# Kernel tuning notes

Hardware: AMD Instinct MI355X
Metric: run time of the kernel (lower is better)

## Reference

```python
import jax, jax.numpy as jnp
import numpy as np

B, IMG, P, C_IN, D, NH, DEPTH, E, TOPK, NCLS = 8, 224, 16, 3, 768, 12, 12, 8, 2, 1000
DH = 4 * D
HD = D // NH
GRID = IMG // P
NPAT = GRID * GRID
MOE_POS = (1, 3, 5, 7, 9, 11)
N_DENSE = DEPTH - len(MOE_POS)
N_MOE = len(MOE_POS)


def setup_inputs() -> dict:
    key = jax.random.key(0)
    ks = iter(jax.random.split(key, 32))
    n = lambda shape: jax.random.normal(next(ks), shape, jnp.float32) * 0.02
    return dict(
        x=jax.random.normal(next(ks), (B, C_IN, IMG, IMG), jnp.float32),
        patch_w=n((D, C_IN * P * P)), patch_b=jnp.zeros((D,), jnp.float32),
        cls_token=n((1, 1, D)), pos_embed=n((1, NPAT + 1, D)),
        ln1_w=jnp.ones((DEPTH, D), jnp.float32), ln1_b=jnp.zeros((DEPTH, D), jnp.float32),
        qkv_w=n((DEPTH, 3 * D, D)), qkv_b=jnp.zeros((DEPTH, 3 * D), jnp.float32),
        proj_w=n((DEPTH, D, D)), proj_b=jnp.zeros((DEPTH, D), jnp.float32),
        ln2_w=jnp.ones((DEPTH, D), jnp.float32), ln2_b=jnp.zeros((DEPTH, D), jnp.float32),
        fc1_w=n((N_DENSE, DH, D)), fc1_b=jnp.zeros((N_DENSE, DH), jnp.float32),
        fc2_w=n((N_DENSE, D, DH)), fc2_b=jnp.zeros((N_DENSE, D), jnp.float32),
        gate_w=n((N_MOE, E, D)), gate_b=jnp.zeros((N_MOE, E), jnp.float32),
        exp_w1=n((N_MOE, E, DH, D)), exp_b1=jnp.zeros((N_MOE, E, DH), jnp.float32),
        exp_w2=n((N_MOE, E, D, DH)), exp_b2=jnp.zeros((N_MOE, E, D), jnp.float32),
        norm_w=jnp.ones((D,), jnp.float32), norm_b=jnp.zeros((D,), jnp.float32),
        head_w=n((NCLS, D)), head_b=jnp.zeros((NCLS,), jnp.float32),
    )


def _ln(x, w, b):
    m = x.mean(-1, keepdims=True)
    v = ((x - m) ** 2).mean(-1, keepdims=True)
    return (x - m) / jnp.sqrt(v + 1e-5) * w + b


def _attn(x, qw, qb, pw, pb):
    Bn, N, _ = x.shape
    qkv = (x @ qw.T + qb).reshape(Bn, N, 3, NH, HD).transpose(2, 0, 3, 1, 4)
    q, k, v = qkv[0], qkv[1], qkv[2]  # [B, NH, N, HD]
    a = jax.nn.softmax(jnp.einsum('bhnd,bhmd->bhnm', q, k) * HD ** -0.5, -1)
    o = jnp.einsum('bhnm,bhmd->bhnd', a, v).transpose(0, 2, 1, 3).reshape(Bn, N, D)
    return o @ pw.T + pb


def _moe(x, gw, gb, w1, b1, w2, b2):
    # FMoETransformerMLP with NaiveGate: top-2 routing, softmax over top-k logits.
    shp = x.shape
    xf = x.reshape(-1, D)  # [T, D]
    logits = xf @ gw.T + gb  # [T, E]
    vals, idx = jax.lax.top_k(logits, TOPK)
    sc = jax.nn.softmax(vals, -1)  # [T, TOPK]
    comb = (jax.nn.one_hot(idx, E, dtype=xf.dtype) * sc[..., None]).sum(1)  # [T, E]
    h = jax.nn.gelu(jnp.einsum('td,ehd->teh', xf, w1) + b1, approximate=False)
    y = jnp.einsum('teh,edh->ted', h, w2) + b2
    return (y * comb[..., None]).sum(1).reshape(shp)


def reference(x, patch_w, patch_b, cls_token, pos_embed, ln1_w, ln1_b, qkv_w, qkv_b, proj_w, proj_b, ln2_w, ln2_b, fc1_w, fc1_b, fc2_w, fc2_b, gate_w, gate_b, exp_w1, exp_b1, exp_w2, exp_b2, norm_w, norm_b, head_w, head_b):
    patches = x.reshape(B, C_IN, GRID, P, GRID, P).transpose(0, 2, 4, 1, 3, 5).reshape(B, NPAT, C_IN * P * P)
    z = jnp.concatenate([jnp.broadcast_to(cls_token, (B, 1, D)), patches @ patch_w.T + patch_b], 1) + pos_embed
    di = mi = 0
    for i in range(DEPTH):
        z = z + _attn(_ln(z, ln1_w[i], ln1_b[i]), qkv_w[i], qkv_b[i], proj_w[i], proj_b[i])
        h2 = _ln(z, ln2_w[i], ln2_b[i])
        if i in MOE_POS:
            z = z + _moe(h2, gate_w[mi], gate_b[mi], exp_w1[mi], exp_b1[mi], exp_w2[mi], exp_b2[mi])
            mi += 1
        else:
            z = z + (jax.nn.gelu(h2 @ fc1_w[di].T + fc1_b[di], approximate=False) @ fc2_w[di].T + fc2_b[di])
            di += 1
    z = _ln(z, norm_w, norm_b)
    return z[:, 0] @ head_w.T + head_b
```

## Files before the change

### kernel.cpp

```cpp
#include <hip/hip_runtime.h>
#include <hip/hip_bf16.h>
#include <math.h>

#define B_     8
#define IMG_   224
#define PATCH_ 16
#define CIN_   3
#define D_     768
#define NH_    12
#define DEPTH_ 12
#define NE_    8
#define NCLS_  1000
#define DH_    3072
#define HD_    64
#define GRD_   14
#define NPAT_  196
#define NTOK_  197
#define T_     (B_*NTOK_)
#define TP_    (B_*NPAT_)
#define NSLOT_ (T_*2)

typedef __bf16 bf16_t;
typedef __bf16 bf16x8 __attribute__((ext_vector_type(8)));
typedef __bf16 bf16x4 __attribute__((ext_vector_type(4)));
typedef float  f32x4  __attribute__((ext_vector_type(4)));

static __device__ __forceinline__ float gelu_f(float x){
    return 0.5f * x * (1.0f + erff(x * 0.70710678118654752440f));
}

__global__ __launch_bounds__(256) void k_cvt(const float* __restrict__ in,
                                             bf16_t* __restrict__ out, int n){
    int i = (blockIdx.x*256 + threadIdx.x)*8;
    if (i >= n) return;
    float4 a = *reinterpret_cast<const float4*>(in + i);
    float4 b = *reinterpret_cast<const float4*>(in + i + 4);
    bf16x8 h;
    h[0]=(bf16_t)a.x; h[1]=(bf16_t)a.y; h[2]=(bf16_t)a.z; h[3]=(bf16_t)a.w;
    h[4]=(bf16_t)b.x; h[5]=(bf16_t)b.y; h[6]=(bf16_t)b.z; h[7]=(bf16_t)b.w;
    *reinterpret_cast<bf16x8*>(out + i) = h;
}

__global__ void k_patch_gather(const float* __restrict__ x, bf16_t* __restrict__ pbuf){
    int idx = blockIdx.x*256 + threadIdx.x;
    if (idx >= TP_*D_) return;
    int k  = idx % D_;
    int tp = idx / D_;
    int p  = tp % NPAT_, b = tp / NPAT_;
    int c  = k >> 8;
    int ij = k & 255;
    int i  = ij >> 4, j = ij & 15;
    int gi = p / GRD_, gj = p % GRD_;
    pbuf[idx] = (bf16_t)x[(((size_t)b*CIN_ + c)*IMG_ + gi*PATCH_ + i)*IMG_ + gj*PATCH_ + j];
}

template<int ACT, int RES, int GATHER, int MOE, int OUTBF>
__global__ __launch_bounds__(256) void k_mgemm(
    const bf16_t* __restrict__ A, const int* __restrict__ gidx,
    const bf16_t* __restrict__ W, const float* __restrict__ bias,
    const float* __restrict__ res, void* __restrict__ Cout,
    int M, int N, int K,
    const int* __restrict__ moff, const int* __restrict__ mcnt)
{
    __shared__ __align__(16) bf16_t As[2][64*64];
    __shared__ __align__(16) bf16_t Bs[2][128*64];
    const int tid = threadIdx.x, lane = tid & 63, w = tid >> 6;
    int row_begin, Mhi;
    if (MOE) {
        const int e = blockIdx.z;
        const int o = moff[e], c = mcnt[e];
        row_begin = o + blockIdx.y*64;
        Mhi = o + c;
        if (row_begin >= Mhi) return;
        W    += (size_t)e*N*K;
        bias += (size_t)e*N;
    } else {
        row_begin = blockIdx.y*64;
        Mhi = M;
    }
    const int bn = blockIdx.x*128;

    const bf16_t* aG[2];
    const bf16_t* wG[4];
    int aOff[2], wOff[4];
    #pragma unroll
    for (int i = 0; i < 2; ++i) {
        const int s = w*2 + i;
        const int row_l = s*8 + (lane >> 3);
        const int cc = (lane & 7) ^ (row_l & 7);
        const int gg = min(row_begin + row_l, Mhi - 1);
        const int tok = GATHER ? (gidx[gg] >> 1) : gg;
        aG[i] = A + (size_t)tok*K + cc*8;
        aOff[i] = s*512;
    }
    #pragma unroll
    for (int j = 0; j < 4; ++j) {
        const int s = w*4 + j;
        const int row_l = s*8 + (lane >> 3);
        const int cc = (lane & 7) ^ (row_l & 7);
        wG[j] = W + (size_t)(bn + row_l)*K + cc*8;
        wOff[j] = s*512;
    }
    const int wm = (w >> 1)*32, wn = (w & 1)*64;
    const int fr = lane & 15, kg = lane >> 4;
    int offA[2][2], offB[2][4];
    #pragma unroll
    for (int ks = 0; ks < 2; ++ks) {
        #pragma unroll
        for (int t = 0; t < 2; ++t) {
            const int ra = wm + t*16 + fr;
            offA[ks][t] = ra*128 + (((ks*4 + kg) ^ (ra & 7)) << 4);
        }
        #pragma unroll
        for (int t = 0; t < 4; ++t) {
            const int rb = wn + t*16 + fr;
            offB[ks][t] = rb*128 + (((ks*4 + kg) ^ (rb & 7)) << 4);
        }
    }

    f32x4 acc[2][4] = {};
    const int nt = K >> 6;
    int cur = 0;
    #pragma unroll
    for (int i = 0; i < 2; ++i) {
        __builtin_amdgcn_global_load_lds(
            (const __attribute__((address_space(1))) void*)(aG[i]),
            (__attribute__((address_space(3))) void*)(&As[0][aOff[i]]), 16, 0, 0);
        aG[i] += 64;
    }
    #pragma unroll
    for (int j = 0; j < 4; ++j) {
        __builtin_amdgcn_global_load_lds(
            (const __attribute__((address_space(1))) void*)(wG[j]),
            (__attribute__((address_space(3))) void*)(&Bs[0][wOff[j]]), 16, 0, 0);
        wG[j] += 64;
    }
    __syncthreads();
    for (int t = 0; t < nt; ++t) {
        if (t + 1 < nt) {
            const int nb = cur ^ 1;
            #pragma unroll
            for (int i = 0; i < 2; ++i) {
                __builtin_amdgcn_global_load_lds(
                    (const __attribute__((address_space(1))) void*)(aG[i]),
                    (__attribute__((address_space(3))) void*)(&As[nb][aOff[i]]), 16, 0, 0);
                aG[i] += 64;
            }
            #pragma unroll
            for (int j = 0; j < 4; ++j) {
                __builtin_amdgcn_global_load_lds(
                    (const __attribute__((address_space(1))) void*)(wG[j]),
                    (__attribute__((address_space(3))) void*)(&Bs[nb][wOff[j]]), 16, 0, 0);
                wG[j] += 64;
            }
        }
        const char* baseA = (const char*)&As[cur][0];
        const char* baseB = (const char*)&Bs[cur][0];
        #pragma unroll
        for (int ks = 0; ks < 2; ++ks) {
            bf16x8 af[2], bf[4];
            #pragma unroll
            for (int t2 = 0; t2 < 2; ++t2)
                af[t2] = *reinterpret_cast<const bf16x8*>(baseA + offA[ks][t2]);
            #pragma unroll
            for (int t2 = 0; t2 < 4; ++t2)
                bf[t2] = *reinterpret_cast<const bf16x8*>(baseB + offB[ks][t2]);
            #pragma unroll
            for (int mt = 0; mt < 2; ++mt)
                #pragma unroll
                for (int nt2 = 0; nt2 < 4; ++nt2)
                    acc[mt][nt2] = __builtin_amdgcn_mfma_f32_16x16x32_bf16(
                        af[mt], bf[nt2], acc[mt][nt2], 0, 0, 0);
        }
        __syncthreads();
        cur ^= 1;
    }
    float*  Cf = (float*)Cout;
    bf16_t* Cb = (bf16_t*)Cout;
    const int cr = (lane >> 4)*4;
    #pragma unroll
    for (int nt2 = 0; nt2 < 4; ++nt2) {
        const int n = bn + wn + nt2*16 + fr;
        const float bv = bias[n];
        #pragma unroll
        for (int mt = 0; mt < 2; ++mt) {
            #pragma unroll
            for (int r2 = 0; r2 < 4; ++r2) {
                const int m = row_begin + wm + mt*16 + cr + r2;
                if (m < Mhi) {
                    float v = acc[mt][nt2][r2] + bv;
                    if (ACT) v = gelu_f(v);
                    if (RES) v += res[(size_t)m*N + n];
                    if (OUTBF) Cb[(size_t)m*N + n] = (bf16_t)v;
                    else       Cf[(size_t)m*N + n] = v;
                }
            }
        }
    }
}

struct LNOut { float y0, y1, y2; };
static __device__ __forceinline__ LNOut ln_block(float v0, float v1, float v2,
        const float* __restrict__ w, const float* __restrict__ b,
        float* red, int tid)
{
    const int wid = tid >> 6, lane = tid & 63;
    float s = v0 + v1 + v2;
    for (int m=32;m>0;m>>=1) s += __shfl_xor(s, m);
    if (lane == 0) red[wid] = s;
    __syncthreads();
    if (tid == 0) red[4] = (red[0]+red[1]+red[2]+red[3]) * (1.0f/768.0f);
    __syncthreads();
    const float mean = red[4];
    float d0 = v0-mean, d1 = v1-mean, d2 = v2-mean;
    float q = d0*d0 + d1*d1 + d2*d2;
    for (int m=32;m>0;m>>=1) q += __shfl_xor(q, m);
    if (lane == 0) red[wid] = q;
    __syncthreads();
    if (tid == 0) {
        float var = (red[0]+red[1]+red[2]+red[3]) * (1.0f/768.0f);
        red[5] = 1.0f / sqrtf(var + 1e-5f);
    }
    __syncthreads();
    const float rstd = red[5];
    LNOut o;
    o.y0 = d0*rstd*w[tid    ] + b[tid    ];
    o.y1 = d1*rstd*w[tid+256] + b[tid+256];
    o.y2 = d2*rstd*w[tid+512] + b[tid+512];
    return o;
}

template<typename TOUT>
__global__ __launch_bounds__(256) void k_ln(const float* __restrict__ X,
        const float* __restrict__ w, const float* __restrict__ b,
        TOUT* __restrict__ Y, int in_mul)
{
    __shared__ float red[8];
    const int r = blockIdx.x, tid = threadIdx.x;
    const float* xr = X + (size_t)r*in_mul*D_;
    LNOut o = ln_block(xr[tid], xr[tid+256], xr[tid+512], w, b, red, tid);
    TOUT* yr = Y + (size_t)r*D_;
    yr[tid] = (TOUT)o.y0; yr[tid+256] = (TOUT)o.y1; yr[tid+512] = (TOUT)o.y2;
}

__global__ __launch_bounds__(256) void k_asmln(const float* __restrict__ pe,
        const float* __restrict__ cls, const float* __restrict__ pos,
        float* __restrict__ z, const float* __restrict__ w,
        const float* __restrict__ b, bf16_t* __restrict__ Y)
{
    __shared__ float red[8];
    const int t = blockIdx.x, tid = threadIdx.x;
    const int bb = t / NTOK_, r = t % NTOK_;
    float v[3];
    #pragma unroll
    for (int j = 0; j < 3; ++j) {
        const int n = tid + j*256;
        if (r == 0) v[j] = cls[n] + pos[n];
        else        v[j] = pe[((size_t)bb*NPAT_ + (r-1))*D_ + n] + pos[(size_t)r*D_ + n];
        z[(size_t)t*D_ + n] = v[j];
    }
    LNOut o = ln_block(v[0], v[1], v[2], w, b, red, tid);
    bf16_t* yr = Y + (size_t)t*D_;
    yr[tid] = (bf16_t)o.y0; yr[tid+256] = (bf16_t)o.y1; yr[tid+512] = (bf16_t)o.y2;
}

__global__ __launch_bounds__(256) void k_lngate(const float* __restrict__ X,
        const float* __restrict__ w, const float* __restrict__ b,
        const float* __restrict__ gw, const float* __restrict__ gb,
        bf16_t* __restrict__ Y, int* __restrict__ t_e, float* __restrict__ t_sc)
{
    __shared__ float red[8];
    __shared__ float red2[4][8];
    const int t = blockIdx.x, tid = threadIdx.x;
    const int wid = tid >> 6, lane = tid & 63;
    const float* xr = X + (size_t)t*D_;
    LNOut o = ln_block(xr[tid], xr[tid+256], xr[tid+512], w, b, red, tid);
    bf16_t* yr = Y + (size_t)t*D_;
    yr[tid] = (bf16_t)o.y0; yr[tid+256] = (bf16_t)o.y1; yr[tid+512] = (bf16_t)o.y2;
    float p[NE_];
    #pragma unroll
    for (int e = 0; e < NE_; ++e)
        p[e] = o.y0*gw[e*D_+tid] + o.y1*gw[e*D_+tid+256] + o.y2*gw[e*D_+tid+512];
    #pragma unroll
    for (int e = 0; e < NE_; ++e)
        for (int m=32;m>0;m>>=1) p[e] += __shfl_xor(p[e], m);
    if (lane == 0)
        #pragma unroll
        for (int e = 0; e < NE_; ++e) red2[wid][e] = p[e];
    __syncthreads();
    if (tid == 0) {
        float l[NE_];
        #pragma unroll
        for (int e = 0; e < NE_; ++e)
            l[e] = red2[0][e]+red2[1][e]+red2[2][e]+red2[3][e] + gb[e];
        int i0 = 0;
        for (int e = 1; e < NE_; ++e) if (l[e] > l[i0]) i0 = e;
        int i1 = -1;
        for (int e = 0; e < NE_; ++e) if (e != i0 && (i1 < 0 || l[e] > l[i1])) i1 = e;
        float e1 = __expf(l[i1] - l[i0]);
        float s = 1.0f + e1;
        t_e[t*2]   = i0;   t_e[t*2+1]  = i1;
        t_sc[t*2]  = 1.0f/s; t_sc[t*2+1] = e1/s;
    }
}

__global__ __launch_bounds__(256) void k_scansc(const int* __restrict__ t_e,
        int* __restrict__ gidx, int* __restrict__ rg,
        int* __restrict__ offs, int* __restrict__ counts)
{
    __shared__ int h[NE_], o[NE_], c2[NE_];
    const int tid = threadIdx.x;
    if (tid < NE_) h[tid] = 0;
    __syncthreads();
    for (int id = tid; id < NSLOT_; id += 256) atomicAdd(&h[t_e[id]], 1);
    __syncthreads();
    if (tid == 0) {
        int s = 0;
        for (int e = 0; e < NE_; ++e) { o[e] = s; s += h[e]; c2[e] = 0; }
    }
    __syncthreads();
    if (tid < NE_) { offs[tid] = o[tid]; counts[tid] = h[tid]; }
    for (int id = tid; id < NSLOT_; id += 256) {
        int e = t_e[id];
        int pos = atomicAdd(&c2[e], 1);
        int g = o[e] + pos;
        gidx[g] = id;
        rg[id] = g;
    }
}

__global__ __launch_bounds__(256) void k_combln(const float* __restrict__ yb,
        const int* __restrict__ rg, const float* __restrict__ t_sc,
        float* __restrict__ z, const float* __restrict__ w,
        const float* __restrict__ b, bf16_t* __restrict__ Y)
{
    __shared__ float red[8];
    const int t = blockIdx.x, tid = threadIdx.x;
    const int g0 = rg[t*2], g1 = rg[t*2+1];
    const float s0 = t_sc[t*2], s1 = t_sc[t*2+1];
    float v[3];
    #pragma unroll
    for (int j = 0; j < 3; ++j) {
        const int n = tid + j*256;
        float nv = z[(size_t)t*D_+n] + s0*yb[(size_t)g0*D_+n] + s1*yb[(size_t)g1*D_+n];
        z[(size_t)t*D_+n] = nv;
        v[j] = nv;
    }
    LNOut o = ln_block(v[0], v[1], v[2], w, b, red, tid);
    bf16_t* yr = Y + (size_t)t*D_;
    yr[tid] = (bf16_t)o.y0; yr[tid+256] = (bf16_t)o.y1; yr[tid+512] = (bf16_t)o.y2;
}

__global__ void k_combine(const float* __restrict__ yb, const int* __restrict__ rg,
                          const float* __restrict__ t_sc, float* __restrict__ z){
    int idx = blockIdx.x*256 + threadIdx.x;
    if (idx >= T_*D_) return;
    int t = idx / D_, n = idx % D_;
    int g0 = rg[t*2], g1 = rg[t*2+1];
    z[idx] += t_sc[t*2]*yb[(size_t)g0*D_+n] + t_sc[t*2+1]*yb[(size_t)g1*D_+n];
}

__global__ __launch_bounds__(256) void k_attn(const bf16_t* __restrict__ qkv,
                                              bf16_t* __restrict__ out)
{
    __shared__ bf16_t Kl[NTOK_*68];
    __shared__ float  qs[8][64];
    __shared__ bf16_t ps[8][200];
    const int qb = blockIdx.x*8;
    const int h = blockIdx.y, b = blockIdx.z;
    const int tid = threadIdx.x, lane = tid & 63, wid = tid >> 6;
    for (int id = tid; id < NTOK_*8; id += 256) {
        const int m = id >> 3, c = id & 7;
        bf16x8 v = *reinterpret_cast<const bf16x8*>(
            qkv + (size_t)(b*NTOK_+m)*2304 + 768 + h*HD_ + c*8);
        bf16x4 lo = {v[0],v[1],v[2],v[3]}, hi = {v[4],v[5],v[6],v[7]};
        *reinterpret_cast<bf16x4*>(&Kl[m*68 + c*8    ]) = lo;
        *reinterpret_cast<bf16x4*>(&Kl[m*68 + c*8 + 4]) = hi;
    }
    for (int id = tid; id < 512; id += 256) {
        const int qq = id >> 6, d = id & 63;
        const int n = qb + qq;
        qs[qq][d] = (n < NTOK_) ? (float)qkv[(size_t)(b*NTOK_+n)*2304 + h*HD_ + d] : 0.0f;
    }
    __syncthreads();
    const int na = qb + wid, nb = qb + wid + 4;
    const bool va = na < NTOK_, vb = nb < NTOK_;
    if (!va) return;
    float sa[4] = {0,0,0,0}, sb[4] = {0,0,0,0};
    for (int d = 0; d < HD_; d += 4) {
        const f32x4 qa = *reinterpret_cast<const f32x4*>(&qs[wid][d]);
        const f32x4 qv = *reinterpret_cast<const f32x4*>(&qs[wid+4][d]);
        #pragma unroll
        for (int j = 0; j < 4; ++j) {
            const int m = lane + 64*j;
            const int mc = m < NTOK_ ? m : NTOK_-1;
            bf16x4 kv = *reinterpret_cast<const bf16x4*>(&Kl[mc*68 + d]);
            float k0=(float)kv[0], k1=(float)kv[1], k2=(float)kv[2], k3=(float)kv[3];
            sa[j] += qa[0]*k0 + qa[1]*k1 + qa[2]*k2 + qa[3]*k3;
            sb[j] += qv[0]*k0 + qv[1]*k1 + qv[2]*k2 + qv[3]*k3;
        }
    }
    #pragma unroll
    for (int j = 0; j < 4; ++j) {
        const bool ok = (lane + 64*j) < NTOK_;
        sa[j] = ok ? sa[j]*0.125f : -3.0e38f;
        sb[j] = ok ? sb[j]*0.125f : -3.0e38f;
    }
    float mxa = fmaxf(fmaxf(sa[0],sa[1]), fmaxf(sa[2],sa[3]));
    float mxb = fmaxf(fmaxf(sb[0],sb[1]), fmaxf(sb[2],sb[3]));
    for (int m=32;m>0;m>>=1) { mxa = fmaxf(mxa, __shfl_xor(mxa,m)); mxb = fmaxf(mxb, __shfl_xor(mxb,m)); }
    float pa[4], pb[4], suma = 0.0f, sumb = 0.0f;
    #pragma unroll
    for (int j = 0; j < 4; ++j) {
        pa[j] = __expf(sa[j]-mxa); suma += pa[j];
        pb[j] = __expf(sb[j]-mxb); sumb += pb[j];
    }
    for (int m=32;m>0;m>>=1) { suma += __shfl_xor(suma,m); sumb += __shfl_xor(sumb,m); }
    #pragma unroll
    for (int j = 0; j < 4; ++j) {
        const int m = lane + 64*j;
        if (m < NTOK_) {
            ps[wid][m] = (bf16_t)pa[j];
            if (vb) ps[wid+4][m] = (bf16_t)pb[j];
        }
    }
    const float inva = 1.0f/suma, invb = 1.0f/sumb;
    const bf16_t* vbase = qkv + (size_t)b*NTOK_*2304 + 1536 + h*HD_ + lane;
    float aa = 0.0f, ab = 0.0f;
    if (vb) {
        for (int m = 0; m < NTOK_; ++m) {
            const float vv = (float)vbase[(size_t)m*2304];
            aa += (float)ps[wid][m]*vv;
            ab += (float)ps[wid+4][m]*vv;
        }
    } else {
        for (int m = 0; m < NTOK_; ++m)
            aa += (float)ps[wid][m]*(float)vbase[(size_t)m*2304];
    }
    out[(size_t)(b*NTOK_+na)*D_ + h*HD_ + lane] = (bf16_t)(aa*inva);
    if (vb) out[(size_t)(b*NTOK_+nb)*D_ + h*HD_ + lane] = (bf16_t)(ab*invb);
}

__global__ __launch_bounds__(256) void k_head(const float* __restrict__ zn,
        const float* __restrict__ hw, const float* __restrict__ hb,
        float* __restrict__ out)
{
    const int o = blockIdx.x*4 + (threadIdx.x >> 6);
    const int b = blockIdx.y;
    const int lane = threadIdx.x & 63;
    if (o >= NCLS_) return;
    float acc = 0.0f;
    #pragma unroll 4
    for (int k = lane; k < D_; k += 64)
        acc = fmaf(zn[b*D_+k], hw[(size_t)o*D_+k], acc);
    for (int m=32;m>0;m>>=1) acc += __shfl_xor(acc, m);
    if (lane == 0) out[b*NCLS_+o] = acc + hb[o];
}

extern "C" void kernel_launch(void* const* d_in, const int* in_sizes, int n_in,
                              void* d_out, int out_size, void* d_ws, size_t ws_size,
                              hipStream_t stream)
{
    const float* x        = (const float*)d_in[0];
    const float* patch_w  = (const float*)d_in[1];
    const float* patch_b  = (const float*)d_in[2];
    const float* cls_tok  = (const float*)d_in[3];
    const float* pos_emb  = (const float*)d_in[4];
    const float* ln1_w    = (const float*)d_in[5];
    const float* ln1_b    = (const float*)d_in[6];
    const float* qkv_w    = (const float*)d_in[7];
    const float* qkv_b    = (const float*)d_in[8];
    const float* proj_w   = (const float*)d_in[9];
    const float* proj_b   = (const float*)d_in[10];
    const float* ln2_w    = (const float*)d_in[11];
    const float* ln2_b    = (const float*)d_in[12];
    const float* fc1_w    = (const float*)d_in[13];
    const float* fc1_b    = (const float*)d_in[14];
    const float* fc2_w    = (const float*)d_in[15];
    const float* fc2_b    = (const float*)d_in[16];
    const float* gate_w   = (const float*)d_in[17];
    const float* gate_b   = (const float*)d_in[18];
    const float* exp_w1   = (const float*)d_in[19];
    const float* exp_b1   = (const float*)d_in[20];
    const float* exp_w2   = (const float*)d_in[21];
    const float* exp_b2   = (const float*)d_in[22];
    const float* norm_w   = (const float*)d_in[23];
    const float* norm_b   = (const float*)d_in[24];
    const float* head_w   = (const float*)d_in[25];
    const float* head_b   = (const float*)d_in[26];

    char* wsb = (char*)d_ws;
    size_t off_ = 0;
    auto alloc = [&](size_t nelem, size_t esz) -> void* {
        void* p = wsb + off_;
        off_ += ((nelem*esz + 255) / 256) * 256;
        return p;
    };
    float*  z      = (float*) alloc((size_t)T_*D_, 4);
    bf16_t* lnbuf  = (bf16_t*)alloc((size_t)T_*D_, 2);
    bf16_t* qkvbuf = (bf16_t*)alloc((size_t)T_*3*D_, 2);
    bf16_t* abuf   = (bf16_t*)alloc((size_t)T_*D_, 2);
    bf16_t* hid    = (bf16_t*)alloc((size_t)NSLOT_*DH_, 2);
    float*  yb     = (float*) alloc((size_t)NSLOT_*D_, 4);
    float*  t_sc   = (float*) alloc(NSLOT_, 4);
    float*  zn     = (float*) alloc((size_t)B_*D_, 4);
    int*    t_e    = (int*)   alloc(NSLOT_, 4);
    int*    rg     = (int*)   alloc(NSLOT_, 4);
    int*    gidx   = (int*)   alloc(NSLOT_, 4);
    int*    offs   = (int*)   alloc(8, 4);
    int*    counts = (int*)   alloc(8, 4);
    const size_t n_patch = (size_t)D_*D_;
    const size_t n_qkv   = (size_t)DEPTH_*3*D_*D_;
    const size_t n_proj  = (size_t)DEPTH_*D_*D_;
    const size_t n_fc1   = (size_t)6*DH_*D_;
    const size_t n_fc2   = (size_t)6*D_*DH_;
    const size_t n_e1    = (size_t)6*NE_*DH_*D_;
    const size_t n_e2    = (size_t)6*NE_*D_*DH_;
    bf16_t* wb_patch = (bf16_t*)alloc(n_patch, 2);
    bf16_t* wb_qkv   = (bf16_t*)alloc(n_qkv, 2);
    bf16_t* wb_proj  = (bf16_t*)alloc(n_proj, 2);
    bf16_t* wb_fc1   = (bf16_t*)alloc(n_fc1, 2);
    bf16_t* wb_fc2   = (bf16_t*)alloc(n_fc2, 2);
    bf16_t* wb_e1    = (bf16_t*)alloc(n_e1, 2);
    bf16_t* wb_e2    = (bf16_t*)alloc(n_e2, 2);
    bf16_t* pbuf   = hid;
    float*  pout   = yb;

    auto cvt = [&](const float* src, bf16_t* dst, size_t n){
        k_cvt<<<dim3((unsigned)((n/8 + 255)/256)), 256, 0, stream>>>(src, dst, (int)n);
    };
    cvt(patch_w, wb_patch, n_patch);
    cvt(qkv_w,   wb_qkv,   n_qkv);
    cvt(proj_w,  wb_proj,  n_proj);
    cvt(fc1_w,   wb_fc1,   n_fc1);
    cvt(fc2_w,   wb_fc2,   n_fc2);
    cvt(exp_w1,  wb_e1,    n_e1);
    cvt(exp_w2,  wb_e2,    n_e2);

    k_patch_gather<<<dim3((TP_*D_+255)/256), 256, 0, stream>>>(x, pbuf);
    k_mgemm<0,0,0,0,0><<<dim3(D_/128, (TP_+63)/64), 256, 0, stream>>>(
        pbuf, nullptr, wb_patch, patch_b, nullptr, pout, TP_, D_, D_, nullptr, nullptr);
    k_asmln<<<T_, 256, 0, stream>>>(pout, cls_tok, pos_emb, z, ln1_w, ln1_b, lnbuf);

    const int GY = (T_+63)/64;
    int di = 0, mi = 0;
    for (int i = 0; i < DEPTH_; ++i){
        k_mgemm<0,0,0,0,1><<<dim3(3*D_/128, GY), 256, 0, stream>>>(
            lnbuf, nullptr, wb_qkv + (size_t)i*3*D_*D_, qkv_b + (size_t)i*3*D_,
            nullptr, qkvbuf, T_, 3*D_, D_, nullptr, nullptr);
        k_attn<<<dim3((NTOK_+7)/8, NH_, B_), 256, 0, stream>>>(qkvbuf, abuf);
        k_mgemm<0,1,0,0,0><<<dim3(D_/128, GY), 256, 0, stream>>>(
            abuf, nullptr, wb_proj + (size_t)i*D_*D_, proj_b + (size_t)i*D_,
            z, z, T_, D_, D_, nullptr, nullptr);
        if (i & 1){
            k_lngate<<<T_, 256, 0, stream>>>(z, ln2_w + i*D_, ln2_b + i*D_,
                gate_w + (size_t)mi*NE_*D_, gate_b + (size_t)mi*NE_,
                lnbuf, t_e, t_sc);
            k_scansc<<<1, 256, 0, stream>>>(t_e, gidx, rg, offs, counts);
            k_mgemm<1,0,1,1,1><<<dim3(DH_/128, 50, NE_), 256, 0, stream>>>(
                lnbuf, gidx, wb_e1 + (size_t)mi*NE_*DH_*D_, exp_b1 + (size_t)mi*NE_*DH_,
                nullptr, hid, NSLOT_, DH_, D_, offs, counts);
            k_mgemm<0,0,0,1,0><<<dim3(D_/128, 50, NE_), 256, 0, stream>>>(
                hid, nullptr, wb_e2 + (size_t)mi*NE_*D_*DH_, exp_b2 + (size_t)mi*NE_*D_,
                nullptr, yb, NSLOT_, D_, DH_, offs, counts);
            if (i + 1 < DEPTH_) {
                k_combln<<<T_, 256, 0, stream>>>(yb, rg, t_sc, z,
                    ln1_w + (i+1)*D_, ln1_b + (i+1)*D_, lnbuf);
            } else {
                k_combine<<<dim3((T_*D_+255)/256), 256, 0, stream>>>(yb, rg, t_sc, z);
            }
            mi++;
        } else {
            k_ln<bf16_t><<<T_, 256, 0, stream>>>(z, ln2_w + i*D_, ln2_b + i*D_, lnbuf, 1);
            k_mgemm<1,0,0,0,1><<<dim3(DH_/128, GY), 256, 0, stream>>>(
                lnbuf, nullptr, wb_fc1 + (size_t)di*DH_*D_, fc1_b + (size_t)di*DH_,
                nullptr, hid, T_, DH_, D_, nullptr, nullptr);
            k_mgemm<0,1,0,0,0><<<dim3(D_/128, GY), 256, 0, stream>>>(
                hid, nullptr, wb_fc2 + (size_t)di*D_*DH_, fc2_b + (size_t)di*D_,
                z, z, T_, D_, DH_, nullptr, nullptr);
            k_ln<bf16_t><<<T_, 256, 0, stream>>>(z, ln1_w + (i+1)*D_, ln1_b + (i+1)*D_, lnbuf, 1);
            di++;
        }
    }
    k_ln<float><<<B_, 256, 0, stream>>>(z, norm_w, norm_b, zn, NTOK_);
    k_head<<<dim3((NCLS_+3)/4, B_), 256, 0, stream>>>(zn, head_w, head_b, (float*)d_out);
}
```

Before: 2.987 ms.

## Split K across waves and grid for narrow GEMMs, fuse residual into LN

Each block now gives every pair of waves its own half of every 64-wide K tile, so each wave computes a full 64x64 output tile. The two halves are merged through shared memory at the end. The N=768 GEMMs (proj, fc2, expert w2) also get a 2-way grid K-split that writes fp32 partials, and the following add+LN or combine kernel sums the partials, bias and residual. This raises block count for the small-N GEMMs, which had few blocks. In exchange it adds partial-buffer traffic, an extra LDS merge pass and extra sync.

```diff
diff --git a/kernel.cpp b/kernel.cpp
--- a/kernel.cpp
+++ b/kernel.cpp
@@ -54,31 +54,34 @@
     pbuf[idx] = (bf16_t)x[(((size_t)b*CIN_ + c)*IMG_ + gi*PATCH_ + i)*IMG_ + gj*PATCH_ + j];
 }
 
-template<int ACT, int RES, int GATHER, int MOE, int OUTBF>
+template<int ACT, int GATHER, int MOE, int OUTBF, int KSPLIT, int PARTIAL>
 __global__ __launch_bounds__(256) void k_mgemm(
     const bf16_t* __restrict__ A, const int* __restrict__ gidx,
     const bf16_t* __restrict__ W, const float* __restrict__ bias,
-    const float* __restrict__ res, void* __restrict__ Cout,
-    int M, int N, int K,
+    void* __restrict__ Cout, int M, int N, int K,
     const int* __restrict__ moff, const int* __restrict__ mcnt)
 {
     __shared__ __align__(16) bf16_t As[2][64*64];
     __shared__ __align__(16) bf16_t Bs[2][128*64];
     const int tid = threadIdx.x, lane = tid & 63, w = tid >> 6;
-    int row_begin, Mhi;
+    int row_begin, Mhi, ksid;
     if (MOE) {
         const int e = blockIdx.z;
         const int o = moff[e], c = mcnt[e];
-        row_begin = o + blockIdx.y*64;
+        const int rb = (KSPLIT == 2) ? (int)(blockIdx.y >> 1) : (int)blockIdx.y;
+        ksid = (KSPLIT == 2) ? (int)(blockIdx.y & 1) : 0;
+        row_begin = o + rb*64;
         Mhi = o + c;
         if (row_begin >= Mhi) return;
-        W    += (size_t)e*N*K;
-        bias += (size_t)e*N;
+        W += (size_t)e*N*K;
+        if (!PARTIAL) bias += (size_t)e*N;
     } else {
         row_begin = blockIdx.y*64;
+        ksid = (KSPLIT == 2) ? (int)blockIdx.z : 0;
         Mhi = M;
     }
     const int bn = blockIdx.x*128;
+    const int KL = K / KSPLIT;
 
     const bf16_t* aG[2];
     const bf16_t* wG[4];
@@ -90,7 +93,7 @@
         const int cc = (lane & 7) ^ (row_l & 7);
         const int gg = min(row_begin + row_l, Mhi - 1);
         const int tok = GATHER ? (gidx[gg] >> 1) : gg;
-        aG[i] = A + (size_t)tok*K + cc*8;
+        aG[i] = A + (size_t)tok*K + ksid*KL + cc*8;
         aOff[i] = s*512;
     }
     #pragma unroll
@@ -98,28 +101,23 @@
         const int s = w*4 + j;
         const int row_l = s*8 + (lane >> 3);
         const int cc = (lane & 7) ^ (row_l & 7);
-        wG[j] = W + (size_t)(bn + row_l)*K + cc*8;
+        wG[j] = W + (size_t)(bn + row_l)*K + ksid*KL + cc*8;
         wOff[j] = s*512;
     }
-    const int wm = (w >> 1)*32, wn = (w & 1)*64;
+    const int kslice = w >> 1, nhalf = w & 1;
     const int fr = lane & 15, kg = lane >> 4;
-    int offA[2][2], offB[2][4];
-    #pragma unroll
-    for (int ks = 0; ks < 2; ++ks) {
-        #pragma unroll
-        for (int t = 0; t < 2; ++t) {
-            const int ra = wm + t*16 + fr;
-            offA[ks][t] = ra*128 + (((ks*4 + kg) ^ (ra & 7)) << 4);
-        }
-        #pragma unroll
-        for (int t = 0; t < 4; ++t) {
-            const int rb = wn + t*16 + fr;
-            offB[ks][t] = rb*128 + (((ks*4 + kg) ^ (rb & 7)) << 4);
-        }
-    }
-
-    f32x4 acc[2][4] = {};
-    const int nt = K >> 6;
+    const int cc0 = kslice*4 + kg;
+    int offA[4], offB[4];
+    #pragma unroll
+    for (int t = 0; t < 4; ++t) {
+        const int ra = t*16 + fr;
+        const int rb2 = nhalf*64 + t*16 + fr;
+        offA[t] = ra*128 + ((cc0 ^ (ra & 7)) << 4);
+        offB[t] = rb2*128 + ((cc0 ^ (rb2 & 7)) << 4);
+    }
+
+    f32x4 acc[4][4] = {};
+    const int nt = KL >> 6;
     int cur = 0;
     #pragma unroll
     for (int i = 0; i < 2; ++i) {
@@ -156,43 +154,56 @@
         }
         const char* baseA = (const char*)&As[cur][0];
         const char* baseB = (const char*)&Bs[cur][0];
-        #pragma unroll
-        for (int ks = 0; ks < 2; ++ks) {
-            bf16x8 af[2], bf[4];
-            #pragma unroll
-            for (int t2 = 0; t2 < 2; ++t2)
-                af[t2] = *reinterpret_cast<const bf16x8*>(baseA + offA[ks][t2]);
-            #pragma unroll
-            for (int t2 = 0; t2 < 4; ++t2)
-                bf[t2] = *reinterpret_cast<const bf16x8*>(baseB + offB[ks][t2]);
-            #pragma unroll
-            for (int mt = 0; mt < 2; ++mt)
-                #pragma unroll
-                for (int nt2 = 0; nt2 < 4; ++nt2)
-                    acc[mt][nt2] = __builtin_amdgcn_mfma_f32_16x16x32_bf16(
-                        af[mt], bf[nt2], acc[mt][nt2], 0, 0, 0);
-        }
+        bf16x8 af[4], bf[4];
+        #pragma unroll
+        for (int t2 = 0; t2 < 4; ++t2) {
+            af[t2] = *reinterpret_cast<const bf16x8*>(baseA + offA[t2]);
+            bf[t2] = *reinterpret_cast<const bf16x8*>(baseB + offB[t2]);
+        }
+        #pragma unroll
+        for (int mt = 0; mt < 4; ++mt)
+            #pragma unroll
+            for (int nt2 = 0; nt2 < 4; ++nt2)
+                acc[mt][nt2] = __builtin_amdgcn_mfma_f32_16x16x32_bf16(
+                    af[mt], bf[nt2], acc[mt][nt2], 0, 0, 0);
         __syncthreads();
         cur ^= 1;
     }
-    float*  Cf = (float*)Cout;
-    bf16_t* Cb = (bf16_t*)Cout;
-    const int cr = (lane >> 4)*4;
-    #pragma unroll
-    for (int nt2 = 0; nt2 < 4; ++nt2) {
-        const int n = bn + wn + nt2*16 + fr;
-        const float bv = bias[n];
-        #pragma unroll
-        for (int mt = 0; mt < 2; ++mt) {
-            #pragma unroll
-            for (int r2 = 0; r2 < 4; ++r2) {
-                const int m = row_begin + wm + mt*16 + cr + r2;
-                if (m < Mhi) {
-                    float v = acc[mt][nt2][r2] + bv;
-                    if (ACT) v = gelu_f(v);
-                    if (RES) v += res[(size_t)m*N + n];
-                    if (OUTBF) Cb[(size_t)m*N + n] = (bf16_t)v;
-                    else       Cf[(size_t)m*N + n] = v;
+    char* mergeBuf = (char*)&Bs[0][0];
+    if (kslice == 1) {
+        char* dst = mergeBuf + nhalf*16384;
+        #pragma unroll
+        for (int mt = 0; mt < 4; ++mt)
+            #pragma unroll
+            for (int nt2 = 0; nt2 < 4; ++nt2)
+                *reinterpret_cast<f32x4*>(dst + (mt*4+nt2)*1024 + lane*16) = acc[mt][nt2];
+    }
+    __syncthreads();
+    if (kslice == 0) {
+        const char* src = mergeBuf + nhalf*16384;
+        #pragma unroll
+        for (int mt = 0; mt < 4; ++mt)
+            #pragma unroll
+            for (int nt2 = 0; nt2 < 4; ++nt2)
+                acc[mt][nt2] += *reinterpret_cast<const f32x4*>(src + (mt*4+nt2)*1024 + lane*16);
+        float*  Cf = (float*)Cout + (PARTIAL ? (size_t)ksid*M*N : (size_t)0);
+        bf16_t* Cb = (bf16_t*)Cout;
+        const int cr = kg*4;
+        #pragma unroll
+        for (int nt2 = 0; nt2 < 4; ++nt2) {
+            const int n = bn + nhalf*64 + nt2*16 + fr;
+            const float bv = PARTIAL ? 0.0f : bias[n];
+            #pragma unroll
+            for (int mt = 0; mt < 4; ++mt) {
+                #pragma unroll
+                for (int r2 = 0; r2 < 4; ++r2) {
+                    const int m = row_begin + mt*16 + cr + r2;
+                    if (m < Mhi) {
+                        float v = acc[mt][nt2][r2] + bv;
+                        if (ACT) v = gelu_f(v);
+                        if (OUTBF) Cb[(size_t)m*N + n] = (bf16_t)v;
+                        else       Cf[(size_t)m*N + n] = v;
+                    }
                 }
             }
         }
@@ -264,47 +275,61 @@
     yr[tid] = (bf16_t)o.y0; yr[tid+256] = (bf16_t)o.y1; yr[tid+512] = (bf16_t)o.y2;
 }
 
-__global__ __launch_bounds__(256) void k_lngate(const float* __restrict__ X,
-        const float* __restrict__ w, const float* __restrict__ b,
-        const float* __restrict__ gw, const float* __restrict__ gb,
-        bf16_t* __restrict__ Y, int* __restrict__ t_e, float* __restrict__ t_sc)
+template<int GATE>
+__global__ __launch_bounds__(256) void k_addln(
+    float* __restrict__ z, const float* __restrict__ P,
+    const float* __restrict__ bias,
+    const float* __restrict__ w, const float* __restrict__ b,
+    bf16_t* __restrict__ Y,
+    const float* __restrict__ gw, const float* __restrict__ gb,
+    int* __restrict__ t_e, float* __restrict__ t_sc)
 {
     __shared__ float red[8];
     __shared__ float red2[4][8];
     const int t = blockIdx.x, tid = threadIdx.x;
     const int wid = tid >> 6, lane = tid & 63;
-    const float* xr = X + (size_t)t*D_;
-    LNOut o = ln_block(xr[tid], xr[tid+256], xr[tid+512], w, b, red, tid);
+    const float* P1 = P + (size_t)T_*D_;
+    float v[3];
+    #pragma unroll
+    for (int j = 0; j < 3; ++j) {
+        const int n = tid + j*256;
+        float nv = z[(size_t)t*D_+n] + P[(size_t)t*D_+n] + P1[(size_t)t*D_+n] + bias[n];
+        z[(size_t)t*D_+n] = nv;
+        v[j] = nv;
+    }
+    LNOut o = ln_block(v[0], v[1], v[2], w, b, red, tid);
     bf16_t* yr = Y + (size_t)t*D_;
     yr[tid] = (bf16_t)o.y0; yr[tid+256] = (bf16_t)o.y1; yr[tid+512] = (bf16_t)o.y2;
-    float p[NE_];
-    #pragma unroll
-    for (int e = 0; e < NE_; ++e)
-        p[e] = o.y0*gw[e*D_+tid] + o.y1*gw[e*D_+tid+256] + o.y2*gw[e*D_+tid+512];
-    #pragma unroll
-    for (int e = 0; e < NE_; ++e)
-        for (int m=32;m>0;m>>=1) p[e] += __shfl_xor(p[e], m);
-    if (lane == 0)
-        #pragma unroll
-        for (int e = 0; e < NE_; ++e) red2[wid][e] = p[e];
-    __syncthreads();
-    if (tid == 0) {
-        float l[NE_];
+    if (GATE) {
+        float p[NE_];
         #pragma unroll
         for (int e = 0; e < NE_; ++e)
-            l[e] = red2[0][e]+red2[1][e]+red2[2][e]+red2[3][e] + gb[e];
-        int i0 = 0;
-        for (int e = 1; e < NE_; ++e) if (l[e] > l[i0]) i0 = e;
-        int i1 = -1;
-        for (int e = 0; e < NE_; ++e) if (e != i0 && (i1 < 0 || l[e] > l[i1])) i1 = e;
-        float e1 = __expf(l[i1] - l[i0]);
-        float s = 1.0f + e1;
-        t_e[t*2]   = i0;   t_e[t*2+1]  = i1;
-        t_sc[t*2]  = 1.0f/s; t_sc[t*2+1] = e1/s;
-    }
-}
-
-__global__ __launch_bounds__(256) void k_scansc(const int* __restrict__ t_e,
+            p[e] = o.y0*gw[e*D_+tid] + o.y1*gw[e*D_+tid+256] + o.y2*gw[e*D_+tid+512];
+        #pragma unroll
+        for (int e = 0; e < NE_; ++e)
+            for (int m=32;m>0;m>>=1) p[e] += __shfl_xor(p[e], m);
+        if (lane == 0)
+            #pragma unroll
+            for (int e = 0; e < NE_; ++e) red2[wid][e] = p[e];
+        __syncthreads();
+        if (tid == 0) {
+            float l[NE_];
+            #pragma unroll
+            for (int e = 0; e < NE_; ++e)
+                l[e] = red2[0][e]+red2[1][e]+red2[2][e]+red2[3][e] + gb[e];
+            int i0 = 0;
+            for (int e = 1; e < NE_; ++e) if (l[e] > l[i0]) i0 = e;
+            int i1 = -1;
+            for (int e = 0; e < NE_; ++e) if (e != i0 && (i1 < 0 || l[e] > l[i1])) i1 = e;
+            float e1 = __expf(l[i1] - l[i0]);
+            float s = 1.0f + e1;
+            t_e[t*2]   = i0;   t_e[t*2+1]  = i1;
+            t_sc[t*2]  = 1.0f/s; t_sc[t*2+1] = e1/s;
+        }
+    }
+}
+
+__global__ __launch_bounds__(1024) void k_scansc(const int* __restrict__ t_e,
         int* __restrict__ gidx, int* __restrict__ rg,
         int* __restrict__ offs, int* __restrict__ counts)
 {
@@ -312,7 +337,7 @@
     const int tid = threadIdx.x;
     if (tid < NE_) h[tid] = 0;
     __syncthreads();
-    for (int id = tid; id < NSLOT_; id += 256) atomicAdd(&h[t_e[id]], 1);
+    for (int id = tid; id < NSLOT_; id += 1024) atomicAdd(&h[t_e[id]], 1);
     __syncthreads();
     if (tid == 0) {
         int s = 0;
@@ -320,7 +345,7 @@
     }
     __syncthreads();
     if (tid < NE_) { offs[tid] = o[tid]; counts[tid] = h[tid]; }
-    for (int id = tid; id < NSLOT_; id += 256) {
+    for (int id = tid; id < NSLOT_; id += 1024) {
         int e = t_e[id];
         int pos = atomicAdd(&c2[e], 1);
         int g = o[e] + pos;
@@ -329,35 +354,35 @@
     }
 }
 
-__global__ __launch_bounds__(256) void k_combln(const float* __restrict__ yb,
-        const int* __restrict__ rg, const float* __restrict__ t_sc,
-        float* __restrict__ z, const float* __restrict__ w,
-        const float* __restrict__ b, bf16_t* __restrict__ Y)
+template<int LN>
+__global__ __launch_bounds__(256) void k_comb(
+    const float* __restrict__ mp, const float* __restrict__ b2,
+    const int* __restrict__ t_e, const int* __restrict__ rg,
+    const float* __restrict__ t_sc, float* __restrict__ z,
+    const float* __restrict__ w, const float* __restrict__ b,
+    bf16_t* __restrict__ Y)
 {
     __shared__ float red[8];
     const int t = blockIdx.x, tid = threadIdx.x;
-    const int g0 = rg[t*2], g1 = rg[t*2+1];
-    const float s0 = t_sc[t*2], s1 = t_sc[t*2+1];
+    const int g0 = rg[2*t], g1 = rg[2*t+1];
+    const int e0 = t_e[2*t], e1 = t_e[2*t+1];
+    const float s0 = t_sc[2*t], s1 = t_sc[2*t+1];
+    const float* mp1 = mp + (size_t)NSLOT_*D_;
     float v[3];
     #pragma unroll
     for (int j = 0; j < 3; ++j) {
         const int n = tid + j*256;
-        float nv = z[(size_t)t*D_+n] + s0*yb[(size_t)g0*D_+n] + s1*yb[(size_t)g1*D_+n];
+        float y0 = mp[(size_t)g0*D_+n] + mp1[(size_t)g0*D_+n] + b2[(size_t)e0*D_+n];
+        float y1 = mp[(size_t)g1*D_+n] + mp1[(size_t)g1*D_+n] + b2[(size_t)e1*D_+n];
+        float nv = z[(size_t)t*D_+n] + s0*y0 + s1*y1;
         z[(size_t)t*D_+n] = nv;
         v[j] = nv;
     }
-    LNOut o = ln_block(v[0], v[1], v[2], w, b, red, tid);
-    bf16_t* yr = Y + (size_t)t*D_;
-    yr[tid] = (bf16_t)o.y0; yr[tid+256] = (bf16_t)o.y1; yr[tid+512] = (bf16_t)o.y2;
-}
-
-__global__ void k_combine(const float* __restrict__ yb, const int* __restrict__ rg,
-                          const float* __restrict__ t_sc, float* __restrict__ z){
-    int idx = blockIdx.x*256 + threadIdx.x;
-    if (idx >= T_*D_) return;
-    int t = idx / D_, n = idx % D_;
-    int g0 = rg[t*2], g1 = rg[t*2+1];
-    z[idx] += t_sc[t*2]*yb[(size_t)g0*D_+n] + t_sc[t*2+1]*yb[(size_t)g1*D_+n];
+    if (LN) {
+        LNOut o = ln_block(v[0], v[1], v[2], w, b, red, tid);
+        bf16_t* yr = Y + (size_t)t*D_;
+        yr[tid] = (bf16_t)o.y0; yr[tid+256] = (bf16_t)o.y1; yr[tid+512] = (bf16_t)o.y2;
+    }
 }
 
 __global__ __launch_bounds__(256) void k_attn(const bf16_t* __restrict__ qkv,
@@ -501,7 +526,8 @@
     bf16_t* qkvbuf = (bf16_t*)alloc((size_t)T_*3*D_, 2);
     bf16_t* abuf   = (bf16_t*)alloc((size_t)T_*D_, 2);
     bf16_t* hid    = (bf16_t*)alloc((size_t)NSLOT_*DH_, 2);
-    float*  yb     = (float*) alloc((size_t)NSLOT_*D_, 4);
+    float*  pp     = (float*) alloc((size_t)2*T_*D_, 4);
+    float*  mp     = (float*) alloc((size_t)2*NSLOT_*D_, 4);
     float*  t_sc   = (float*) alloc(NSLOT_, 4);
     float*  zn     = (float*) alloc((size_t)B_*D_, 4);
     int*    t_e    = (int*)   alloc(NSLOT_, 4);
@@ -524,7 +550,7 @@
     bf16_t* wb_e1    = (bf16_t*)alloc(n_e1, 2);
     bf16_t* wb_e2    = (bf16_t*)alloc(n_e2, 2);
     bf16_t* pbuf   = hid;
-    float*  pout   = yb;
+    float*  pout   = mp;
 
     auto cvt = [&](const float* src, bf16_t* dst, size_t n){
         k_cvt<<<dim3((unsigned)((n/8 + 255)/256)), 256, 0, stream>>>(src, dst, (int)n);
@@ -538,47 +564,52 @@
     cvt(exp_w2,  wb_e2,    n_e2);
 
     k_patch_gather<<<dim3((TP_*D_+255)/256), 256, 0, stream>>>(x, pbuf);
-    k_mgemm<0,0,0,0,0><<<dim3(D_/128, (TP_+63)/64), 256, 0, stream>>>(
-        pbuf, nullptr, wb_patch, patch_b, nullptr, pout, TP_, D_, D_, nullptr, nullptr);
+    k_mgemm<0,0,0,0,1,0><<<dim3(D_/128, (TP_+63)/64), 256, 0, stream>>>(
+        pbuf, nullptr, wb_patch, patch_b, pout, TP_, D_, D_, nullptr, nullptr);
     k_asmln<<<T_, 256, 0, stream>>>(pout, cls_tok, pos_emb, z, ln1_w, ln1_b, lnbuf);
 
     const int GY = (T_+63)/64;
     int di = 0, mi = 0;
     for (int i = 0; i < DEPTH_; ++i){
-        k_mgemm<0,0,0,0,1><<<dim3(3*D_/128, GY), 256, 0, stream>>>(
+        k_mgemm<0,0,0,1,1,0><<<dim3(3*D_/128, GY), 256, 0, stream>>>(
             lnbuf, nullptr, wb_qkv + (size_t)i*3*D_*D_, qkv_b + (size_t)i*3*D_,
-            nullptr, qkvbuf, T_, 3*D_, D_, nullptr, nullptr);
+            qkvbuf, T_, 3*D_, D_, nullptr, nullptr);
         k_attn<<<dim3((NTOK_+7)/8, NH_, B_), 256, 0, stream>>>(qkvbuf, abuf);
-        k_mgemm<0,1,0,0,0><<<dim3(D_/128, GY), 256, 0, stream>>>(
-            abuf, nullptr, wb_proj + (size_t)i*D_*D_, proj_b + (size_t)i*D_,
-            z, z, T_, D_, D_, nullptr, nullptr);
+        k_mgemm<0,0,0,0,2,1><<<dim3(D_/128, GY, 2), 256, 0, stream>>>(
+            abuf, nullptr, wb_proj + (size_t)i*D_*D_, nullptr,
+            pp, T_, D_, D_, nullptr, nullptr);
         if (i & 1){
-            k_lngate<<<T_, 256, 0, stream>>>(z, ln2_w + i*D_, ln2_b + i*D_,
-                gate_w + (size_t)mi*NE_*D_, gate_b + (size_t)mi*NE_,
-                lnbuf, t_e, t_sc);
-            k_scansc<<<1, 256, 0, stream>>>(t_e, gidx, rg, offs, counts);
-            k_mgemm<1,0,1,1,1><<<dim3(DH_/128, 50, NE_), 256, 0, stream>>>(
+            k_addln<1><<<T_, 256, 0, stream>>>(z, pp, proj_b + i*D_,
+                ln2_w + i*D_, ln2_b + i*D_, lnbuf,
+                gate_w + (size_t)mi*NE_*D_, gate_b + (size_t)mi*NE_, t_e, t_sc);
+            k_scansc<<<1, 1024, 0, stream>>>(t_e, gidx, rg, offs, counts);
+            k_mgemm<1,1,1,1,1,0><<<dim3(DH_/128, 50, NE_), 256, 0, stream>>>(
                 lnbuf, gidx, wb_e1 + (size_t)mi*NE_*DH_*D_, exp_b1 + (size_t)mi*NE_*DH_,
-                nullptr, hid, NSLOT_, DH_, D_, offs, counts);
-            k_mgemm<0,0,0,1,0><<<dim3(D_/128, 50, NE_), 256, 0, stream>>>(
-                hid, nullptr, wb_e2 + (size_t)mi*NE_*D_*DH_, exp_b2 + (size_t)mi*NE_*D_,
-                nullptr, yb, NSLOT_, D_, DH_, offs, counts);
+                hid, NSLOT_, DH_, D_, offs, counts);
+            k_mgemm<0,0,1,0,2,1><<<dim3(D_/128, 100, NE_), 256, 0, stream>>>(
+                hid, nullptr, wb_e2 + (size_t)mi*NE_*D_*DH_, nullptr,
+                mp, NSLOT_, D_, DH_, offs, counts);
             if (i + 1 < DEPTH_) {
-                k_combln<<<T_, 256, 0, stream>>>(yb, rg, t_sc, z,
-                    ln1_w + (i+1)*D_, ln1_b + (i+1)*D_, lnbuf);
+                k_comb<1><<<T_, 256, 0, stream>>>(mp, exp_b2 + (size_t)mi*NE_*D_,
+                    t_e, rg, t_sc, z, ln1_w + (i+1)*D_, ln1_b + (i+1)*D_, lnbuf);
             } else {
-                k_combine<<<dim3((T_*D_+255)/256), 256, 0, stream>>>(yb, rg, t_sc, z);
+                k_comb<0><<<T_, 256, 0, stream>>>(mp, exp_b2 + (size_t)mi*NE_*D_,
+                    t_e, rg, t_sc, z, nullptr, nullptr, nullptr);
             }
             mi++;
         } else {
-            k_ln<bf16_t><<<T_, 256, 0, stream>>>(z, ln2_w + i*D_, ln2_b + i*D_, lnbuf, 1);
-            k_mgemm<1,0,0,0,1><<<dim3(DH_/128, GY), 256, 0, stream>>>(
+            k_addln<0><<<T_, 256, 0, stream>>>(z, pp, proj_b + i*D_,
+                ln2_w + i*D_, ln2_b + i*D_, lnbuf,
+                nullptr, nullptr, nullptr, nullptr);
+            k_mgemm<1,0,0,1,1,0><<<dim3(DH_/128, GY), 256, 0, stream>>>(
                 lnbuf, nullptr, wb_fc1 + (size_t)di*DH_*D_, fc1_b + (size_t)di*DH_,
-                nullptr, hid, T_, DH_, D_, nullptr, nullptr);
-            k_mgemm<0,1,0,0,0><<<dim3(D_/128, GY), 256, 0, stream>>>(
-                hid, nullptr, wb_fc2 + (size_t)di*D_*DH_, fc2_b + (size_t)di*D_,
-                z, z, T_, D_, DH_, nullptr, nullptr);
-            k_ln<bf16_t><<<T_, 256, 0, stream>>>(z, ln1_w + (i+1)*D_, ln1_b + (i+1)*D_, lnbuf, 1);
+                hid, T_, DH_, D_, nullptr, nullptr);
+            k_mgemm<0,0,0,0,2,1><<<dim3(D_/128, GY, 2), 256, 0, stream>>>(
+                hid, nullptr, wb_fc2 + (size_t)di*D_*DH_, nullptr,
+                pp, T_, D_, DH_, nullptr, nullptr);
+            k_addln<0><<<T_, 256, 0, stream>>>(z, pp, fc2_b + di*D_,
+                ln1_w + (i+1)*D_, ln1_b + (i+1)*D_, lnbuf,
+                nullptr, nullptr, nullptr, nullptr);
             di++;
         }
     }
```

New measurement: 3.180 ms. +6.4%, slower.
